# Optimization experiments

Hardware: AMD Instinct MI355X
Metric: run time of the kernel (lower is better)

## Reference

```python
import jax, jax.numpy as jnp
import numpy as np

N_NODES = 100000
N_EDGES = 3200000
STATE_DIM = 128
ACTION_DIM = 8


def _w(key, shape, scale=0.05):
    return (jax.random.normal(key, shape, dtype=jnp.float32) * scale)


def setup_inputs() -> dict:
    key = jax.random.key(0)
    ks = jax.random.split(key, 24)
    x = jax.random.normal(ks[0], (N_NODES, STATE_DIM), dtype=jnp.float32)
    edge_index = jax.random.randint(ks[1], (2, N_EDGES), 0, N_NODES, dtype=jnp.int64)
    inp = {
        "x": x,
        "edge_index": edge_index,
        # GCN layers (weights stored [in, out] so forward is x @ W + b)
        "W1": _w(ks[2], (STATE_DIM, 128)), "b1": jnp.zeros((128,), jnp.float32),
        "W2": _w(ks[3], (128, 128)),       "b2": jnp.zeros((128,), jnp.float32),
        "W3": _w(ks[4], (128, 64)),        "b3": jnp.zeros((64,), jnp.float32),
        # actor MLP 64->128->64->ACTION_DIM + softmax
        "Wa1": _w(ks[5], (64, 128)),  "ba1": jnp.zeros((128,), jnp.float32),
        "Wa2": _w(ks[6], (128, 64)),  "ba2": jnp.zeros((64,), jnp.float32),
        "Wa3": _w(ks[7], (64, ACTION_DIM)), "ba3": jnp.zeros((ACTION_DIM,), jnp.float32),
        # critic MLP 64->128->64->1
        "Wc1": _w(ks[8], (64, 128)),  "bc1": jnp.zeros((128,), jnp.float32),
        "Wc2": _w(ks[9], (128, 64)),  "bc2": jnp.zeros((64,), jnp.float32),
        "Wc3": _w(ks[10], (64, 1)),   "bc3": jnp.zeros((1,), jnp.float32),
    }
    return inp


def _gcn_conv(x, W, b, src, dst, norm):
    # GCNConv: D^{-1/2} (A + I) D^{-1/2} X W + b  (self loops already in src/dst)
    h = x @ W                                   # [N, out]
    msg = h[src] * norm[:, None]                # gather + per-edge scale
    agg = jax.ops.segment_sum(msg, dst, num_segments=N_NODES)
    return agg + b


def reference(x, edge_index,
              W1, b1, W2, b2, W3, b3,
              Wa1, ba1, Wa2, ba2, Wa3, ba3,
              Wc1, bc1, Wc2, bc2, Wc3, bc3):
    loop = jnp.arange(N_NODES, dtype=edge_index.dtype)
    src = jnp.concatenate([edge_index[0], loop])
    dst = jnp.concatenate([edge_index[1], loop])
    deg = jax.ops.segment_sum(jnp.ones_like(dst, dtype=x.dtype), dst,
                              num_segments=N_NODES)
    dinv = jax.lax.rsqrt(deg)                   # deg >= 1 via self loops
    norm = dinv[src] * dinv[dst]                # [E+N]

    # forward_gnn (dropout is identity in eval mode)
    h = jax.nn.relu(_gcn_conv(x, W1, b1, src, dst, norm))
    h = jax.nn.relu(_gcn_conv(h, W2, b2, src, dst, norm))
    h = _gcn_conv(h, W3, b3, src, dst, norm)    # [N, 64]

    a = jax.nn.relu(h @ Wa1 + ba1)
    a = jax.nn.relu(a @ Wa2 + ba2)
    probs = jax.nn.softmax(a @ Wa3 + ba3, axis=-1)   # [N, ACTION_DIM]

    c = jax.nn.relu(h @ Wc1 + bc1)
    c = jax.nn.relu(c @ Wc2 + bc2)
    values = c @ Wc3 + bc3                      # [N, 1]

    return jnp.concatenate([probs, values], axis=-1)  # [N, ACTION_DIM+1]
```

## Files before the change

kernel.cpp:

```cpp
#include <hip/hip_runtime.h>
#include <hip/hip_bf16.h>
#include <math.h>


#define WS_ALIGN(x) (((x) + 255) & ~(size_t)255)

constexpr int RNG    = 8;
constexpr int CHK    = 32;
constexpr int NRG_SZ = 12500;
constexpr int NB_A   = 256;

constexpr float S_FP8     = 64.0f;
constexpr float S_FP8_INV = 1.0f / 64.0f;

using bf16x8 = __attribute__((ext_vector_type(8))) short;
using f32x4  = __attribute__((ext_vector_type(4))) float;
using f32x2  = __attribute__((ext_vector_type(2))) float;

__device__ __forceinline__ float b2f(unsigned short u) {
    return __uint_as_float(((unsigned int)u) << 16);
}
__device__ __forceinline__ unsigned short f2b(float f) {
    __hip_bfloat16 hb = __float2bfloat16(f);
    return *(unsigned short*)&hb;
}
__device__ __forceinline__ unsigned char f2fp8(float f) {
    return (unsigned char)(__builtin_amdgcn_cvt_pk_fp8_f32(f, f, 0, false) & 0xff);
}
__device__ __forceinline__ int pad8(int v) { return (v + 7) & ~7; }


__global__ __launch_bounds__(256) void bucket_count_k(
    const int* __restrict__ dst, int* __restrict__ bcnt, int E) {
    __shared__ int c8[RNG];
    int b = blockIdx.x, t = threadIdx.x;
    if (t < RNG) c8[t] = 0;
    __syncthreads();
    int ec = (E + NB_A - 1) / NB_A;
    int e0 = b * ec, e1 = min(E, e0 + ec);
    for (int e = e0 + t; e < e1; e += 256) {
        int d = __builtin_nontemporal_load(dst + e);
        atomicAdd(&c8[d / NRG_SZ], 1);
    }
    __syncthreads();
    if (t < RNG) bcnt[t * NB_A + b] = c8[t];
}

__global__ void bucket_off_k(const int* __restrict__ bcnt, int* __restrict__ base,
                             int* __restrict__ bstart, int E) {
    __shared__ int s[RNG * NB_A];
    int t = threadIdx.x;
    s[t] = bcnt[t];
    s[t + 1024] = bcnt[t + 1024];
    __syncthreads();
    if (t == 0) {
        int run = 0;
        for (int i = 0; i < RNG * NB_A; i++) { int v = s[i]; s[i] = run; run += v; }
    }
    __syncthreads();
    base[t] = s[t];
    base[t + 1024] = s[t + 1024];
    if (t < RNG) bstart[t] = s[t * NB_A];
    if (t == 0) bstart[RNG] = E;
}

__global__ __launch_bounds__(256) void bucket_scatter_k(
    const int* __restrict__ src, const int* __restrict__ dst,
    const int* __restrict__ base, unsigned long long* __restrict__ bucket, int E) {
    __shared__ int cur[RNG];
    int b = blockIdx.x, t = threadIdx.x;
    if (t < RNG) cur[t] = base[t * NB_A + b];
    __syncthreads();
    int ec = (E + NB_A - 1) / NB_A;
    int e0 = b * ec, e1 = min(E, e0 + ec);
    for (int e = e0 + t; e < e1; e += 256) {
        int d = __builtin_nontemporal_load(dst + e);
        int sv = __builtin_nontemporal_load(src + e);
        int r = d / NRG_SZ;
        int pos = atomicAdd(&cur[r], 1);
        bucket[pos] = ((unsigned long long)(d - r * NRG_SZ) << 32) | (unsigned int)sv;
    }
}

__global__ __launch_bounds__(256) void hist_bucket_k(
    const unsigned long long* __restrict__ bucket, const int* __restrict__ bstart,
    int* __restrict__ hist) {
    __shared__ int h[NRG_SZ];
    int b = blockIdx.x, r = b & 7, c2 = b >> 3, t = threadIdx.x;
    for (int i = t; i < NRG_SZ; i += 256) h[i] = 0;
    int s0 = bstart[r], s1 = bstart[r + 1];
    int ec = (s1 - s0 + CHK - 1) / CHK;
    int e0 = s0 + c2 * ec, e1 = min(s1, e0 + ec);
    __syncthreads();
    for (int e = e0 + t; e < e1; e += 256) {
        unsigned long long v = __builtin_nontemporal_load(bucket + e);
        atomicAdd(&h[(int)(v >> 32)], 1);
    }
    __syncthreads();
    int* out = hist + ((size_t)r * CHK + c2) * NRG_SZ;
    for (int i = t; i < NRG_SZ; i += 256) out[i] = h[i];
}

__global__ void sum_hist_dinv_k(const int* __restrict__ hist, int* __restrict__ cnt,
                                float* __restrict__ dinv, int N) {
    int i = blockIdx.x * 256 + threadIdx.x;
    if (i >= N) return;
    int r = i / NRG_SZ, li = i - r * NRG_SZ;
    const int* hp = hist + ((size_t)r * CHK) * NRG_SZ + li;
    int s = 0;
#pragma unroll
    for (int c = 0; c < CHK; c++) s += hp[(size_t)c * NRG_SZ];
    cnt[i] = s;
    dinv[i] = rsqrtf((float)s + 1.0f);
}

__global__ void chunk_sum_k(const int* __restrict__ cnt, int* __restrict__ bsum, int n) {
    __shared__ int sd[256];
    int t = threadIdx.x;
    int i = blockIdx.x * 256 + t;
    sd[t] = (i < n) ? pad8(cnt[i]) : 0;
    __syncthreads();
    for (int d = 128; d > 0; d >>= 1) {
        if (t < d) sd[t] += sd[t + d];
        __syncthreads();
    }
    if (t == 0) bsum[blockIdx.x] = sd[0];
}

__global__ void scan_mid_k(const int* __restrict__ bsum, int* __restrict__ boff,
                           int nb, int* __restrict__ rowptr, int N) {
    __shared__ int s[512];
    int t = threadIdx.x;
    s[t] = (t < nb) ? bsum[t] : 0;
    __syncthreads();
    if (t == 0) {
        int run = 0;
        for (int i = 0; i < nb; i++) { int v = s[i]; s[i] = run; run += v; }
        rowptr[N] = run;
    }
    __syncthreads();
    if (t < nb) boff[t] = s[t];
}

__global__ void scan_final_k(const int* __restrict__ cnt, const int* __restrict__ boff,
                             int* __restrict__ rowptr, int n) {
    __shared__ int s[256];
    int t = threadIdx.x;
    int i = blockIdx.x * 256 + t;
    int v = (i < n) ? pad8(cnt[i]) : 0;
    s[t] = v;
    __syncthreads();
    for (int d = 1; d < 256; d <<= 1) {
        int x = (t >= d) ? s[t - d] : 0;
        __syncthreads();
        s[t] += x;
        __syncthreads();
    }
    if (i < n) rowptr[i] = s[t] - v + boff[blockIdx.x];
}

__global__ void offsets_k(int* __restrict__ hist, const int* __restrict__ rowptr, int N) {
    int i = blockIdx.x * 256 + threadIdx.x;
    if (i >= N) return;
    int r = i / NRG_SZ, li = i - r * NRG_SZ;
    int* hp = hist + ((size_t)r * CHK) * NRG_SZ + li;
    int run = rowptr[i];
#pragma unroll
    for (int c = 0; c < CHK; c++) {
        int v = hp[(size_t)c * NRG_SZ];
        hp[(size_t)c * NRG_SZ] = run;
        run += v;
    }
}

__global__ __launch_bounds__(256) void fill2_k(
    const unsigned long long* __restrict__ bucket, const int* __restrict__ bstart,
    const int* __restrict__ hist, int* __restrict__ col) {
    __shared__ int cur[NRG_SZ];
    int b = blockIdx.x, r = b & 7, c2 = b >> 3, t = threadIdx.x;
    const int* hp = hist + ((size_t)r * CHK + c2) * NRG_SZ;
    for (int i = t; i < NRG_SZ; i += 256) cur[i] = hp[i];
    int s0 = bstart[r], s1 = bstart[r + 1];
    int ec = (s1 - s0 + CHK - 1) / CHK;
    int e0 = s0 + c2 * ec, e1 = min(s1, e0 + ec);
    __syncthreads();
    for (int e = e0 + t; e < e1; e += 256) {
        unsigned long long v = __builtin_nontemporal_load(bucket + e);
        int slot = atomicAdd(&cur[(int)(v >> 32)], 1);
        col[slot] = (int)(unsigned int)(v & 0xffffffffULL);
    }
}

__global__ void pad_col_k(const int* __restrict__ cnt, const int* __restrict__ rowptr,
                          int* __restrict__ col, int N) {
    int i = blockIdx.x * 256 + threadIdx.x;
    if (i >= N) return;
    int e = rowptr[i] + cnt[i], end = rowptr[i + 1];
    for (; e < end; e++) col[e] = N;
}


__global__ __launch_bounds__(256) void prep_w_k(
    const float* __restrict__ W1, const float* __restrict__ W2,
    const float* __restrict__ W3, const float* __restrict__ Wa1,
    const float* __restrict__ Wa2, const float* __restrict__ Wc1,
    const float* __restrict__ Wc2, unsigned short* __restrict__ wt) {
    int i = blockIdx.x * 256 + threadIdx.x;
    const float* W; int off, K, OUT;
    if (i < 16384)      { W = W1;  off = 0;     K = 128; OUT = 128; }
    else if (i < 32768) { W = W2;  off = 16384; K = 128; OUT = 128; }
    else if (i < 40960) { W = W3;  off = 32768; K = 128; OUT = 64; }
    else if (i < 49152) { W = Wa1; off = 40960; K = 64;  OUT = 128; }
    else if (i < 57344) { W = Wa2; off = 49152; K = 128; OUT = 64; }
    else if (i < 65536) { W = Wc1; off = 57344; K = 64;  OUT = 128; }
    else                { W = Wc2; off = 65536; K = 128; OUT = 64; }
    int j = i - off, k = j / OUT, n = j - k * OUT;
    wt[off + n * K + k] = f2b(W[j]);
}


template <int K, int OUT, bool AF32, bool BIAS_RELU, bool OFP8>
__global__ __launch_bounds__(256) void gemm_mfma_k(
    const void* __restrict__ Xv, const unsigned short* __restrict__ Wt,
    const float* __restrict__ sb,
    void* __restrict__ Yv, int N) {
    constexpr int LDK = K + 8;
    __shared__ __align__(16) unsigned short As[64 * LDK];
    __shared__ __align__(16) unsigned short Bs[OUT * LDK];
    int t = threadIdx.x;
    int rowBase = blockIdx.x * 64;

    if constexpr (AF32) {
        const float* X = (const float*)Xv;
        for (int g = t; g < 64 * (K / 8); g += 256) {
            int r = g / (K / 8), q = g - r * (K / 8);
            int gr = rowBase + r;
            unsigned short us[8];
            if (gr < N) {
                float4 v0 = *(const float4*)(X + (size_t)gr * K + q * 8);
                float4 v1 = *(const float4*)(X + (size_t)gr * K + q * 8 + 4);
                us[0] = f2b(v0.x); us[1] = f2b(v0.y); us[2] = f2b(v0.z); us[3] = f2b(v0.w);
                us[4] = f2b(v1.x); us[5] = f2b(v1.y); us[6] = f2b(v1.z); us[7] = f2b(v1.w);
            } else {
#pragma unroll
                for (int j = 0; j < 8; j++) us[j] = 0;
            }
            *(uint4*)&As[r * LDK + q * 8] = *(uint4*)us;
        }
    } else {
        const unsigned short* X = (const unsigned short*)Xv;
        for (int g = t; g < 64 * (K / 8); g += 256) {
            int r = g / (K / 8), q = g - r * (K / 8);
            int gr = rowBase + r;
            uint4 v = make_uint4(0, 0, 0, 0);
            if (gr < N) v = *(const uint4*)(X + (size_t)gr * K + q * 8);
            *(uint4*)&As[r * LDK + q * 8] = v;
        }
    }
    for (int g = t; g < OUT * (K / 8); g += 256) {
        int r = g / (K / 8), q = g - r * (K / 8);
        *(uint4*)&Bs[r * LDK + q * 8] = *(const uint4*)(Wt + r * K + q * 8);
    }
    __syncthreads();

    int wv = t >> 6, lane = t & 63;
    int lm = lane & 15, lq = lane >> 4;
    constexpr int CT = OUT / 16;
    f32x4 acc[CT];
#pragma unroll
    for (int c = 0; c < CT; c++) acc[c] = (f32x4){0.f, 0.f, 0.f, 0.f};

    const unsigned short* arow = &As[(wv * 16 + lm) * LDK + lq * 8];
#pragma unroll
    for (int kt = 0; kt < K / 32; kt++) {
        bf16x8 a = *(const bf16x8*)(arow + kt * 32);
#pragma unroll
        for (int c = 0; c < CT; c++) {
            bf16x8 b = *(const bf16x8*)&Bs[(c * 16 + lm) * LDK + kt * 32 + lq * 8];
            acc[c] = __builtin_amdgcn_mfma_f32_16x16x32_bf16(a, b, acc[c], 0, 0, 0);
        }
    }

    int r0 = rowBase + wv * 16 + lq * 4;
#pragma unroll
    for (int r = 0; r < 4; r++) {
        int gr = r0 + r;
        if constexpr (OFP8) {
            float scale = (gr < N) ? sb[gr] * S_FP8 : 0.f;
#pragma unroll
            for (int c = 0; c < CT; c++) {
                int colg = c * 16 + lm;
                ((unsigned char*)Yv)[(size_t)gr * OUT + colg] = f2fp8(acc[c][r] * scale);
            }
        } else if (gr < N) {
#pragma unroll
            for (int c = 0; c < CT; c++) {
                int colg = c * 16 + lm;
                float v = acc[c][r];
                if constexpr (BIAS_RELU) v = fmaxf(v + sb[colg], 0.f);
                else v = v * sb[gr];
                ((unsigned short*)Yv)[(size_t)gr * OUT + colg] = f2b(v);
            }
        }
    }
}


template <bool RELU>
__global__ __launch_bounds__(256) void agg128_k(
    const unsigned char* __restrict__ H,
    const int* __restrict__ rowptr, const int* __restrict__ col,
    const float* __restrict__ dinv, const float* __restrict__ bias,
    unsigned short* __restrict__ Y, int N, int Ecap) {
    int tid = threadIdx.x;
    int node = blockIdx.x * 4 + (tid >> 6);
    if (node >= N) return;
    int lane = tid & 63;
    int half = lane >> 5;
    int li4 = (lane & 31) * 4;

    float acc0 = 0.f, acc1 = 0.f, acc2 = 0.f, acc3 = 0.f;
    if (half == 0) {
        unsigned u = *(const unsigned*)(H + (size_t)node * 128 + li4);
        f32x2 lo = __builtin_amdgcn_cvt_pk_f32_fp8((int)u, false);
        f32x2 hi = __builtin_amdgcn_cvt_pk_f32_fp8((int)u, true);
        acc0 = lo[0]; acc1 = lo[1]; acc2 = hi[0]; acc3 = hi[1];
    }

    int start = rowptr[node], end = rowptr[node + 1];
    for (int e0 = start; e0 < end; e0 += 64) {
        int cidx = e0 + lane;
        int cv = col[min(cidx, Ecap - 1)];
        int pairs = min(64, end - e0) >> 1;
        for (int p = 0; p < pairs; p += 4) {
            int s0 = __shfl(cv, 2 * p + half, 64);
            int s1 = __shfl(cv, 2 * p + 2 + half, 64);
            int s2 = __shfl(cv, 2 * p + 4 + half, 64);
            int s3 = __shfl(cv, 2 * p + 6 + half, 64);
            unsigned u0 = *(const unsigned*)(H + (size_t)s0 * 128 + li4);
            unsigned u1 = *(const unsigned*)(H + (size_t)s1 * 128 + li4);
            unsigned u2 = *(const unsigned*)(H + (size_t)s2 * 128 + li4);
            unsigned u3 = *(const unsigned*)(H + (size_t)s3 * 128 + li4);
            f32x2 a0 = __builtin_amdgcn_cvt_pk_f32_fp8((int)u0, false);
            f32x2 b0 = __builtin_amdgcn_cvt_pk_f32_fp8((int)u0, true);
            f32x2 a1 = __builtin_amdgcn_cvt_pk_f32_fp8((int)u1, false);
            f32x2 b1 = __builtin_amdgcn_cvt_pk_f32_fp8((int)u1, true);
            f32x2 a2 = __builtin_amdgcn_cvt_pk_f32_fp8((int)u2, false);
            f32x2 b2 = __builtin_amdgcn_cvt_pk_f32_fp8((int)u2, true);
            f32x2 a3 = __builtin_amdgcn_cvt_pk_f32_fp8((int)u3, false);
            f32x2 b3 = __builtin_amdgcn_cvt_pk_f32_fp8((int)u3, true);
            acc0 += (a0[0] + a1[0]) + (a2[0] + a3[0]);
            acc1 += (a0[1] + a1[1]) + (a2[1] + a3[1]);
            acc2 += (b0[0] + b1[0]) + (b2[0] + b3[0]);
            acc3 += (b0[1] + b1[1]) + (b2[1] + b3[1]);
        }
    }

    acc0 += __shfl_xor(acc0, 32, 64);
    acc1 += __shfl_xor(acc1, 32, 64);
    acc2 += __shfl_xor(acc2, 32, 64);
    acc3 += __shfl_xor(acc3, 32, 64);

    if (half == 0) {
        float dv = dinv[node] * S_FP8_INV;
        float4 bb = *(const float4*)(bias + li4);
        float o0 = acc0 * dv + bb.x, o1 = acc1 * dv + bb.y;
        float o2 = acc2 * dv + bb.z, o3 = acc3 * dv + bb.w;
        if (RELU) {
            o0 = fmaxf(o0, 0.f); o1 = fmaxf(o1, 0.f);
            o2 = fmaxf(o2, 0.f); o3 = fmaxf(o3, 0.f);
        }
        ushort4 st = make_ushort4(f2b(o0), f2b(o1), f2b(o2), f2b(o3));
        *(ushort4*)(Y + (size_t)node * 128 + li4) = st;
    }
}

__global__ __launch_bounds__(256) void agg64_k(
    const unsigned char* __restrict__ H,
    const int* __restrict__ rowptr, const int* __restrict__ col,
    const float* __restrict__ dinv, const float* __restrict__ bias,
    unsigned short* __restrict__ Y, int N, int Ecap) {
    int tid = threadIdx.x;
    int node = blockIdx.x * 4 + (tid >> 6);
    if (node >= N) return;
    int lane = tid & 63;
    int quarter = lane >> 4;
    int li4 = (lane & 15) * 4;

    float acc0 = 0.f, acc1 = 0.f, acc2 = 0.f, acc3 = 0.f;
    if (quarter == 0) {
        unsigned u = *(const unsigned*)(H + (size_t)node * 64 + li4);
        f32x2 lo = __builtin_amdgcn_cvt_pk_f32_fp8((int)u, false);
        f32x2 hi = __builtin_amdgcn_cvt_pk_f32_fp8((int)u, true);
        acc0 = lo[0]; acc1 = lo[1]; acc2 = hi[0]; acc3 = hi[1];
    }

    int start = rowptr[node], end = rowptr[node + 1];
    for (int e0 = start; e0 < end; e0 += 64) {
        int cidx = e0 + lane;
        int cv = col[min(cidx, Ecap - 1)];
        int quads = min(64, end - e0) >> 2;
        for (int q = 0; q < quads; q += 2) {
            int s0 = __shfl(cv, 4 * q + quarter, 64);
            int s1 = __shfl(cv, 4 * q + 4 + quarter, 64);
            unsigned u0 = *(const unsigned*)(H + (size_t)s0 * 64 + li4);
            unsigned u1 = *(const unsigned*)(H + (size_t)s1 * 64 + li4);
            f32x2 a0 = __builtin_amdgcn_cvt_pk_f32_fp8((int)u0, false);
            f32x2 b0 = __builtin_amdgcn_cvt_pk_f32_fp8((int)u0, true);
            f32x2 a1 = __builtin_amdgcn_cvt_pk_f32_fp8((int)u1, false);
            f32x2 b1 = __builtin_amdgcn_cvt_pk_f32_fp8((int)u1, true);
            acc0 += a0[0] + a1[0];
            acc1 += a0[1] + a1[1];
            acc2 += b0[0] + b1[0];
            acc3 += b0[1] + b1[1];
        }
    }

    acc0 += __shfl_xor(acc0, 16, 64); acc0 += __shfl_xor(acc0, 32, 64);
    acc1 += __shfl_xor(acc1, 16, 64); acc1 += __shfl_xor(acc1, 32, 64);
    acc2 += __shfl_xor(acc2, 16, 64); acc2 += __shfl_xor(acc2, 32, 64);
    acc3 += __shfl_xor(acc3, 16, 64); acc3 += __shfl_xor(acc3, 32, 64);

    if (quarter == 0 && (lane >> 5) == 0) {
        float dv = dinv[node] * S_FP8_INV;
        float4 bb = *(const float4*)(bias + li4);
        ushort4 st = make_ushort4(f2b(acc0 * dv + bb.x), f2b(acc1 * dv + bb.y),
                                  f2b(acc2 * dv + bb.z), f2b(acc3 * dv + bb.w));
        *(ushort4*)(Y + (size_t)node * 64 + li4) = st;
    }
}


__global__ __launch_bounds__(256) void logits_k(
    const unsigned short* __restrict__ A2,
    const unsigned short* __restrict__ C2,
    const float* __restrict__ Wa3, const float* __restrict__ ba3,
    const float* __restrict__ Wc3, const float* __restrict__ bc3,
    float* __restrict__ out, int N) {
    int t = threadIdx.x;
    int node = blockIdx.x * 32 + (t >> 3);
    int a = t & 7;
    if (node >= N) return;

    const unsigned short* ar = A2 + (size_t)node * 64;
    float s = ba3[a];
#pragma unroll
    for (int q = 0; q < 8; q++) {
        uint4 pv = *(const uint4*)(ar + q * 8);
        const unsigned short* pu = (const unsigned short*)&pv;
#pragma unroll
        for (int j = 0; j < 8; j++)
            s = fmaf(b2f(pu[j]), Wa3[(q * 8 + j) * 8 + a], s);
    }
    float m = s;
#pragma unroll
    for (int w = 1; w < 8; w <<= 1) m = fmaxf(m, __shfl_xor(m, w, 64));
    float e = expf(s - m);
    float sum = e;
#pragma unroll
    for (int w = 1; w < 8; w <<= 1) sum += __shfl_xor(sum, w, 64);
    out[(size_t)node * 9 + a] = e / sum;

    if (a == 0) {
        const unsigned short* cr = C2 + (size_t)node * 64;
        float v = bc3[0];
#pragma unroll
        for (int q = 0; q < 8; q++) {
            uint4 pv = *(const uint4*)(cr + q * 8);
            const unsigned short* pu = (const unsigned short*)&pv;
#pragma unroll
            for (int j = 0; j < 8; j++)
                v = fmaf(b2f(pu[j]), Wc3[q * 8 + j], v);
        }
        out[(size_t)node * 9 + 8] = v;
    }
}


extern "C" void kernel_launch(void* const* d_in, const int* in_sizes, int n_in,
                              void* d_out, int out_size, void* d_ws, size_t ws_size,
                              hipStream_t stream) {
    const float* x   = (const float*)d_in[0];
    const int*   ei  = (const int*)d_in[1];
    const float* W1  = (const float*)d_in[2];  const float* b1  = (const float*)d_in[3];
    const float* W2  = (const float*)d_in[4];  const float* b2  = (const float*)d_in[5];
    const float* W3  = (const float*)d_in[6];  const float* b3  = (const float*)d_in[7];
    const float* Wa1 = (const float*)d_in[8];  const float* ba1 = (const float*)d_in[9];
    const float* Wa2 = (const float*)d_in[10]; const float* ba2 = (const float*)d_in[11];
    const float* Wa3 = (const float*)d_in[12]; const float* ba3 = (const float*)d_in[13];
    const float* Wc1 = (const float*)d_in[14]; const float* bc1 = (const float*)d_in[15];
    const float* Wc2 = (const float*)d_in[16]; const float* bc2 = (const float*)d_in[17];
    const float* Wc3 = (const float*)d_in[18]; const float* bc3 = (const float*)d_in[19];
    float* out = (float*)d_out;

    const int N = in_sizes[0] / 128;
    const int E = in_sizes[1] / 2;
    const int* src = ei;
    const int* dst = ei + E;
    const int Ecap = E + 8 * N;
    const int Npad = ((N + 63) / 64) * 64;

    size_t off = 0;
    auto take = [&](size_t bytes) { size_t o = off; off = WS_ALIGN(off + bytes); return o; };
    char* ws = (char*)d_ws;
    unsigned short* h      = (unsigned short*)(ws + take((size_t)N * 128 * 2));
    unsigned char*  hpr8   = (unsigned char*) (ws + take((size_t)(Npad + 64) * 128));
    unsigned short* h3     = (unsigned short*)(ws + take((size_t)N * 64 * 2));
    int*            col    = (int*)(ws + take((size_t)Ecap * 4));
    unsigned short* A1C1   = (unsigned short*)(ws + take((size_t)N * 128 * 2));
    unsigned short* wt     = (unsigned short*)(ws + take(73728 * 2));
    float* dinv   = (float*)(ws + take((size_t)(N + 64) * 4));
    int*   cnt    = (int*)  (ws + take((size_t)N * 4));
    int*   rowptr = (int*)  (ws + take((size_t)(N + 1) * 4));
    int*   bcnt   = (int*)  (ws + take(RNG * NB_A * 4));
    int*   base   = (int*)  (ws + take(RNG * NB_A * 4));
    int*   bstart = (int*)  (ws + take((RNG + 1) * 4));
    int*   bsum   = (int*)  (ws + take(512 * 4));
    int*   boff   = (int*)  (ws + take(512 * 4));
    unsigned long long* bucket = (unsigned long long*)h;
    int* hist = (int*)A1C1;
    unsigned short* A2 = (unsigned short*)col;
    unsigned short* C2 = (unsigned short*)hpr8;
    (void)ws_size; (void)n_in; (void)out_size;

    const int nb  = (N + 255) / 256;
    const int gN  = (N + 255) / 256;
    const int gT  = (N + 63) / 64;

    prep_w_k<<<288, 256, 0, stream>>>(W1, W2, W3, Wa1, Wa2, Wc1, Wc2, wt);
    const unsigned short* W1t  = wt;
    const unsigned short* W2t  = wt + 16384;
    const unsigned short* W3t  = wt + 32768;
    const unsigned short* Wa1t = wt + 40960;
    const unsigned short* Wa2t = wt + 49152;
    const unsigned short* Wc1t = wt + 57344;
    const unsigned short* Wc2t = wt + 65536;

    bucket_count_k<<<NB_A, 256, 0, stream>>>(dst, bcnt, E);
    bucket_off_k<<<1, 1024, 0, stream>>>(bcnt, base, bstart, E);
    bucket_scatter_k<<<NB_A, 256, 0, stream>>>(src, dst, base, bucket, E);
    hist_bucket_k<<<RNG * CHK, 256, 0, stream>>>(bucket, bstart, hist);
    sum_hist_dinv_k<<<gN, 256, 0, stream>>>(hist, cnt, dinv, N);
    chunk_sum_k<<<nb, 256, 0, stream>>>(cnt, bsum, N);
    scan_mid_k<<<1, 512, 0, stream>>>(bsum, boff, nb, rowptr, N);
    scan_final_k<<<nb, 256, 0, stream>>>(cnt, boff, rowptr, N);
    offsets_k<<<gN, 256, 0, stream>>>(hist, rowptr, N);
    fill2_k<<<RNG * CHK, 256, 0, stream>>>(bucket, bstart, hist, col);
    pad_col_k<<<gN, 256, 0, stream>>>(cnt, rowptr, col, N);

    gemm_mfma_k<128, 128, true,  false, true><<<gT, 256, 0, stream>>>(x, W1t, dinv, hpr8, N);
    agg128_k<true><<<(N + 3) / 4, 256, 0, stream>>>(hpr8, rowptr, col, dinv, b1, h, N, Ecap);
    gemm_mfma_k<128, 128, false, false, true><<<gT, 256, 0, stream>>>(h, W2t, dinv, hpr8, N);
    agg128_k<true><<<(N + 3) / 4, 256, 0, stream>>>(hpr8, rowptr, col, dinv, b2, h, N, Ecap);
    gemm_mfma_k<128, 64,  false, false, true><<<gT, 256, 0, stream>>>(h, W3t, dinv, hpr8, N);
    agg64_k<<<(N + 3) / 4, 256, 0, stream>>>(hpr8, rowptr, col, dinv, b3, h3, N, Ecap);

    gemm_mfma_k<64,  128, false, true, false><<<gT, 256, 0, stream>>>(h3, Wa1t, ba1, A1C1, N);
    gemm_mfma_k<128, 64,  false, true, false><<<gT, 256, 0, stream>>>(A1C1, Wa2t, ba2, A2, N);
    gemm_mfma_k<64,  128, false, true, false><<<gT, 256, 0, stream>>>(h3, Wc1t, bc1, A1C1, N);
    gemm_mfma_k<128, 64,  false, true, false><<<gT, 256, 0, stream>>>(A1C1, Wc2t, bc2, C2, N);
    logits_k<<<(N + 31) / 32, 256, 0, stream>>>(A2, C2, Wa3, ba3, Wc3, bc3, out, N);
}
```

Baseline: 558.8 us.

## Use finer 64-range CSR bucketing with packed 32-bit keys and wider aggregation loads

```diff
diff --git a/kernel.cpp b/kernel.cpp
--- a/kernel.cpp
+++ b/kernel.cpp
@@ -5,10 +5,10 @@
 
 #define WS_ALIGN(x) (((x) + 255) & ~(size_t)255)
 
-constexpr int RNG    = 8;
-constexpr int CHK    = 32;
-constexpr int NRG_SZ = 12500;
-constexpr int NB_A   = 256;
+constexpr int RNG  = 64;
+constexpr int NRG  = 1563;
+constexpr int NB   = 1024;
+constexpr int CHK  = 16;
 
 constexpr float S_FP8     = 64.0f;
 constexpr float S_FP8_INV = 1.0f / 64.0f;
@@ -29,87 +29,109 @@
 }
 __device__ __forceinline__ int pad8(int v) { return (v + 7) & ~7; }
 
+__device__ __forceinline__ void acc8(uint2 u, f32x2& a01, f32x2& a23,
+                                     f32x2& a45, f32x2& a67) {
+    a01 += __builtin_amdgcn_cvt_pk_f32_fp8((int)u.x, false);
+    a23 += __builtin_amdgcn_cvt_pk_f32_fp8((int)u.x, true);
+    a45 += __builtin_amdgcn_cvt_pk_f32_fp8((int)u.y, false);
+    a67 += __builtin_amdgcn_cvt_pk_f32_fp8((int)u.y, true);
+}
+
 
 __global__ __launch_bounds__(256) void bucket_count_k(
     const int* __restrict__ dst, int* __restrict__ bcnt, int E) {
-    __shared__ int c8[RNG];
+    __shared__ int c64[RNG];
     int b = blockIdx.x, t = threadIdx.x;
-    if (t < RNG) c8[t] = 0;
-    __syncthreads();
-    int ec = (E + NB_A - 1) / NB_A;
+    if (t < RNG) c64[t] = 0;
+    __syncthreads();
+    int ec = (E + NB - 1) / NB;
     int e0 = b * ec, e1 = min(E, e0 + ec);
     for (int e = e0 + t; e < e1; e += 256) {
         int d = __builtin_nontemporal_load(dst + e);
-        atomicAdd(&c8[d / NRG_SZ], 1);
-    }
-    __syncthreads();
-    if (t < RNG) bcnt[t * NB_A + b] = c8[t];
-}
-
-__global__ void bucket_off_k(const int* __restrict__ bcnt, int* __restrict__ base,
-                             int* __restrict__ bstart, int E) {
-    __shared__ int s[RNG * NB_A];
-    int t = threadIdx.x;
-    s[t] = bcnt[t];
-    s[t + 1024] = bcnt[t + 1024];
-    __syncthreads();
-    if (t == 0) {
+        atomicAdd(&c64[d / NRG], 1);
+    }
+    __syncthreads();
+    if (t < RNG) bcnt[t * NB + b] = c64[t];
+}
+
+__global__ __launch_bounds__(256) void rsum_k(
+    const int* __restrict__ bcnt, int* __restrict__ base, int* __restrict__ rtot) {
+    __shared__ int s[256];
+    int r = blockIdx.x, t = threadIdx.x;
+    const int* row = bcnt + (size_t)r * NB;
+    int v[4], loc = 0;
+#pragma unroll
+    for (int j = 0; j < 4; j++) { v[j] = row[t * 4 + j]; loc += v[j]; }
+    s[t] = loc;
+    __syncthreads();
+    for (int d = 1; d < 256; d <<= 1) {
+        int x = (t >= d) ? s[t - d] : 0;
+        __syncthreads();
+        s[t] += x;
+        __syncthreads();
+    }
+    int run = s[t] - loc;
+    int* bp = base + (size_t)r * NB + t * 4;
+#pragma unroll
+    for (int j = 0; j < 4; j++) { bp[j] = run; run += v[j]; }
+    if (t == 255) rtot[r] = s[255];
+}
+
+__global__ void rstart_k(const int* __restrict__ rtot, int* __restrict__ bstart) {
+    if (threadIdx.x == 0) {
         int run = 0;
-        for (int i = 0; i < RNG * NB_A; i++) { int v = s[i]; s[i] = run; run += v; }
-    }
-    __syncthreads();
-    base[t] = s[t];
-    base[t + 1024] = s[t + 1024];
-    if (t < RNG) bstart[t] = s[t * NB_A];
-    if (t == 0) bstart[RNG] = E;
+        for (int r = 0; r < RNG; r++) { bstart[r] = run; run += rtot[r]; }
+        bstart[RNG] = run;
+    }
 }
 
 __global__ __launch_bounds__(256) void bucket_scatter_k(
     const int* __restrict__ src, const int* __restrict__ dst,
-    const int* __restrict__ base, unsigned long long* __restrict__ bucket, int E) {
+    const int* __restrict__ base, const int* __restrict__ bstart,
+    unsigned* __restrict__ bucket, int E) {
     __shared__ int cur[RNG];
     int b = blockIdx.x, t = threadIdx.x;
-    if (t < RNG) cur[t] = base[t * NB_A + b];
-    __syncthreads();
-    int ec = (E + NB_A - 1) / NB_A;
+    if (t < RNG) cur[t] = bstart[t] + base[(size_t)t * NB + b];
+    __syncthreads();
+    int ec = (E + NB - 1) / NB;
     int e0 = b * ec, e1 = min(E, e0 + ec);
     for (int e = e0 + t; e < e1; e += 256) {
         int d = __builtin_nontemporal_load(dst + e);
         int sv = __builtin_nontemporal_load(src + e);
-        int r = d / NRG_SZ;
+        int r = d / NRG;
         int pos = atomicAdd(&cur[r], 1);
-        bucket[pos] = ((unsigned long long)(d - r * NRG_SZ) << 32) | (unsigned int)sv;
+        bucket[pos] = ((unsigned)(d - r * NRG) << 17) | (unsigned)sv;
     }
 }
 
 __global__ __launch_bounds__(256) void hist_bucket_k(
-    const unsigned long long* __restrict__ bucket, const int* __restrict__ bstart,
+    const unsigned* __restrict__ bucket, const int* __restrict__ bstart,
     int* __restrict__ hist) {
-    __shared__ int h[NRG_SZ];
-    int b = blockIdx.x, r = b & 7, c2 = b >> 3, t = threadIdx.x;
-    for (int i = t; i < NRG_SZ; i += 256) h[i] = 0;
+    __shared__ int h[NRG];
+    int b = blockIdx.x, r = b & 63, c2 = b >> 6, t = threadIdx.x;
+    for (int i = t; i < NRG; i += 256) h[i] = 0;
     int s0 = bstart[r], s1 = bstart[r + 1];
     int ec = (s1 - s0 + CHK - 1) / CHK;
     int e0 = s0 + c2 * ec, e1 = min(s1, e0 + ec);
     __syncthreads();
     for (int e = e0 + t; e < e1; e += 256) {
-        unsigned long long v = __builtin_nontemporal_load(bucket + e);
-        atomicAdd(&h[(int)(v >> 32)], 1);
-    }
-    __syncthreads();
-    int* out = hist + ((size_t)r * CHK + c2) * NRG_SZ;
-    for (int i = t; i < NRG_SZ; i += 256) out[i] = h[i];
+        unsigned v = __builtin_nontemporal_load(bucket + e);
+        atomicAdd(&h[v >> 17], 1);
+    }
+    __syncthreads();
+    int* out = hist + ((size_t)r * CHK + c2) * NRG;
+    for (int i = t; i < NRG; i += 256) out[i] = h[i];
 }
 
 __global__ void sum_hist_dinv_k(const int* __restrict__ hist, int* __restrict__ cnt,
                                 float* __restrict__ dinv, int N) {
     int i = blockIdx.x * 256 + threadIdx.x;
     if (i >= N) return;
-    int r = i / NRG_SZ, li = i - r * NRG_SZ;
-    const int* hp = hist + ((size_t)r * CHK) * NRG_SZ + li;
+    int r = i / NRG, li = i - r * NRG;
+    const int* hp = hist + ((size_t)r * CHK) * NRG + li;
     int s = 0;
 #pragma unroll
-    for (int c = 0; c < CHK; c++) s += hp[(size_t)c * NRG_SZ];
+    for (int c = 0; c < CHK; c++) s += hp[(size_t)c * NRG];
     cnt[i] = s;
     dinv[i] = rsqrtf((float)s + 1.0f);
 }
@@ -162,32 +184,32 @@
 __global__ void offsets_k(int* __restrict__ hist, const int* __restrict__ rowptr, int N) {
     int i = blockIdx.x * 256 + threadIdx.x;
     if (i >= N) return;
-    int r = i / NRG_SZ, li = i - r * NRG_SZ;
-    int* hp = hist + ((size_t)r * CHK) * NRG_SZ + li;
+    int r = i / NRG, li = i - r * NRG;
+    int* hp = hist + ((size_t)r * CHK) * NRG + li;
     int run = rowptr[i];
 #pragma unroll
     for (int c = 0; c < CHK; c++) {
-        int v = hp[(size_t)c * NRG_SZ];
-        hp[(size_t)c * NRG_SZ] = run;
+        int v = hp[(size_t)c * NRG];
+        hp[(size_t)c * NRG] = run;
         run += v;
     }
 }
 
 __global__ __launch_bounds__(256) void fill2_k(
-    const unsigned long long* __restrict__ bucket, const int* __restrict__ bstart,
+    const unsigned* __restrict__ bucket, const int* __restrict__ bstart,
     const int* __restrict__ hist, int* __restrict__ col) {
-    __shared__ int cur[NRG_SZ];
-    int b = blockIdx.x, r = b & 7, c2 = b >> 3, t = threadIdx.x;
-    const int* hp = hist + ((size_t)r * CHK + c2) * NRG_SZ;
-    for (int i = t; i < NRG_SZ; i += 256) cur[i] = hp[i];
+    __shared__ int cur[NRG];
+    int b = blockIdx.x, r = b & 63, c2 = b >> 6, t = threadIdx.x;
+    const int* hp = hist + ((size_t)r * CHK + c2) * NRG;
+    for (int i = t; i < NRG; i += 256) cur[i] = hp[i];
     int s0 = bstart[r], s1 = bstart[r + 1];
     int ec = (s1 - s0 + CHK - 1) / CHK;
     int e0 = s0 + c2 * ec, e1 = min(s1, e0 + ec);
     __syncthreads();
     for (int e = e0 + t; e < e1; e += 256) {
-        unsigned long long v = __builtin_nontemporal_load(bucket + e);
-        int slot = atomicAdd(&cur[(int)(v >> 32)], 1);
-        col[slot] = (int)(unsigned int)(v & 0xffffffffULL);
+        unsigned v = __builtin_nontemporal_load(bucket + e);
+        int slot = atomicAdd(&cur[v >> 17], 1);
+        col[slot] = (int)(v & 0x1FFFFu);
     }
 }
 
@@ -316,62 +338,52 @@
     int node = blockIdx.x * 4 + (tid >> 6);
     if (node >= N) return;
     int lane = tid & 63;
-    int half = lane >> 5;
-    int li4 = (lane & 31) * 4;
-
-    float acc0 = 0.f, acc1 = 0.f, acc2 = 0.f, acc3 = 0.f;
-    if (half == 0) {
-        unsigned u = *(const unsigned*)(H + (size_t)node * 128 + li4);
-        f32x2 lo = __builtin_amdgcn_cvt_pk_f32_fp8((int)u, false);
-        f32x2 hi = __builtin_amdgcn_cvt_pk_f32_fp8((int)u, true);
-        acc0 = lo[0]; acc1 = lo[1]; acc2 = hi[0]; acc3 = hi[1];
+    int grp = lane >> 4;
+    int li8 = (lane & 15) * 8;
+
+    f32x2 a01 = {0.f, 0.f}, a23 = {0.f, 0.f}, a45 = {0.f, 0.f}, a67 = {0.f, 0.f};
+    if (grp == 0) {
+        uint2 u = *(const uint2*)(H + (size_t)node * 128 + li8);
+        acc8(u, a01, a23, a45, a67);
     }
 
     int start = rowptr[node], end = rowptr[node + 1];
     for (int e0 = start; e0 < end; e0 += 64) {
-        int cidx = e0 + lane;
-        int cv = col[min(cidx, Ecap - 1)];
-        int pairs = min(64, end - e0) >> 1;
-        for (int p = 0; p < pairs; p += 4) {
-            int s0 = __shfl(cv, 2 * p + half, 64);
-            int s1 = __shfl(cv, 2 * p + 2 + half, 64);
-            int s2 = __shfl(cv, 2 * p + 4 + half, 64);
-            int s3 = __shfl(cv, 2 * p + 6 + half, 64);
-            unsigned u0 = *(const unsigned*)(H + (size_t)s0 * 128 + li4);
-            unsigned u1 = *(const unsigned*)(H + (size_t)s1 * 128 + li4);
-            unsigned u2 = *(const unsigned*)(H + (size_t)s2 * 128 + li4);
-            unsigned u3 = *(const unsigned*)(H + (size_t)s3 * 128 + li4);
-            f32x2 a0 = __builtin_amdgcn_cvt_pk_f32_fp8((int)u0, false);
-            f32x2 b0 = __builtin_amdgcn_cvt_pk_f32_fp8((int)u0, true);
-            f32x2 a1 = __builtin_amdgcn_cvt_pk_f32_fp8((int)u1, false);
-            f32x2 b1 = __builtin_amdgcn_cvt_pk_f32_fp8((int)u1, true);
-            f32x2 a2 = __builtin_amdgcn_cvt_pk_f32_fp8((int)u2, false);
-            f32x2 b2 = __builtin_amdgcn_cvt_pk_f32_fp8((int)u2, true);
-            f32x2 a3 = __builtin_amdgcn_cvt_pk_f32_fp8((int)u3, false);
-            f32x2 b3 = __builtin_amdgcn_cvt_pk_f32_fp8((int)u3, true);
-            acc0 += (a0[0] + a1[0]) + (a2[0] + a3[0]);
-            acc1 += (a0[1] + a1[1]) + (a2[1] + a3[1]);
-            acc2 += (b0[0] + b1[0]) + (b2[0] + b3[0]);
-            acc3 += (b0[1] + b1[1]) + (b2[1] + b3[1]);
-        }
-    }
-
-    acc0 += __shfl_xor(acc0, 32, 64);
-    acc1 += __shfl_xor(acc1, 32, 64);
-    acc2 += __shfl_xor(acc2, 32, 64);
-    acc3 += __shfl_xor(acc3, 32, 64);
-
-    if (half == 0) {
+        int cv = col[min(e0 + lane, Ecap - 1)];
+        int quads = min(64, end - e0) >> 2;
+        for (int q = 0; q < quads; q += 2) {
+            int s0 = __shfl(cv, 4 * q + grp, 64);
+            int s1 = __shfl(cv, 4 * q + 4 + grp, 64);
+            uint2 u0 = *(const uint2*)(H + (size_t)s0 * 128 + li8);
+            uint2 u1 = *(const uint2*)(H + (size_t)s1 * 128 + li8);
+            acc8(u0, a01, a23, a45, a67);
+            acc8(u1, a01, a23, a45, a67);
+        }
+    }
+
+#pragma unroll
+    for (int w = 16; w < 64; w <<= 1) {
+        a01[0] += __shfl_xor(a01[0], w, 64); a01[1] += __shfl_xor(a01[1], w, 64);
+        a23[0] += __shfl_xor(a23[0], w, 64); a23[1] += __shfl_xor(a23[1], w, 64);
+        a45[0] += __shfl_xor(a45[0], w, 64); a45[1] += __shfl_xor(a45[1], w, 64);
+        a67[0] += __shfl_xor(a67[0], w, 64); a67[1] += __shfl_xor(a67[1], w, 64);
+    }
+
+    if (grp == 0) {
         float dv = dinv[node] * S_FP8_INV;
-        float4 bb = *(const float4*)(bias + li4);
-        float o0 = acc0 * dv + bb.x, o1 = acc1 * dv + bb.y;
-        float o2 = acc2 * dv + bb.z, o3 = acc3 * dv + bb.w;
+        float4 b0 = *(const float4*)(bias + li8);
+        float4 b1 = *(const float4*)(bias + li8 + 4);
+        float o0 = a01[0] * dv + b0.x, o1 = a01[1] * dv + b0.y;
+        float o2 = a23[0] * dv + b0.z, o3 = a23[1] * dv + b0.w;
+        float o4 = a45[0] * dv + b1.x, o5 = a45[1] * dv + b1.y;
+        float o6 = a67[0] * dv + b1.z, o7 = a67[1] * dv + b1.w;
         if (RELU) {
-            o0 = fmaxf(o0, 0.f); o1 = fmaxf(o1, 0.f);
-            o2 = fmaxf(o2, 0.f); o3 = fmaxf(o3, 0.f);
-        }
-        ushort4 st = make_ushort4(f2b(o0), f2b(o1), f2b(o2), f2b(o3));
-        *(ushort4*)(Y + (size_t)node * 128 + li4) = st;
+            o0 = fmaxf(o0, 0.f); o1 = fmaxf(o1, 0.f); o2 = fmaxf(o2, 0.f); o3 = fmaxf(o3, 0.f);
+            o4 = fmaxf(o4, 0.f); o5 = fmaxf(o5, 0.f); o6 = fmaxf(o6, 0.f); o7 = fmaxf(o7, 0.f);
+        }
+        unsigned short us[8] = {f2b(o0), f2b(o1), f2b(o2), f2b(o3),
+                                f2b(o4), f2b(o5), f2b(o6), f2b(o7)};
+        *(uint4*)(Y + (size_t)node * 128 + li8) = *(uint4*)us;
     }
 }
 
@@ -384,49 +396,53 @@
     int node = blockIdx.x * 4 + (tid >> 6);
     if (node >= N) return;
     int lane = tid & 63;
-    int quarter = lane >> 4;
-    int li4 = (lane & 15) * 4;
-
-    float acc0 = 0.f, acc1 = 0.f, acc2 = 0.f, acc3 = 0.f;
-    if (quarter == 0) {
-        unsigned u = *(const unsigned*)(H + (size_t)node * 64 + li4);
-        f32x2 lo = __builtin_amdgcn_cvt_pk_f32_fp8((int)u, false);
-        f32x2 hi = __builtin_amdgcn_cvt_pk_f32_fp8((int)u, true);
-        acc0 = lo[0]; acc1 = lo[1]; acc2 = hi[0]; acc3 = hi[1];
+    int grp = lane >> 3;
+    int li8 = (lane & 7) * 8;
+
+    f32x2 a01 = {0.f, 0.f}, a23 = {0.f, 0.f}, a45 = {0.f, 0.f}, a67 = {0.f, 0.f};
+    if (grp == 0) {
+        uint2 u = *(const uint2*)(H + (size_t)node * 64 + li8);
+        acc8(u, a01, a23, a45, a67);
     }
 
     int start = rowptr[node], end = rowptr[node + 1];
     for (int e0 = start; e0 < end; e0 += 64) {
-        int cidx = e0 + lane;
-        int cv = col[min(cidx, Ecap - 1)];
-        int quads = min(64, end - e0) >> 2;
-        for (int q = 0; q < quads; q += 2) {
-            int s0 = __shfl(cv, 4 * q + quarter, 64);
-            int s1 = __shfl(cv, 4 * q + 4 + quarter, 64);
-            unsigned u0 = *(const unsigned*)(H + (size_t)s0 * 64 + li4);
-            unsigned u1 = *(const unsigned*)(H + (size_t)s1 * 64 + li4);
-            f32x2 a0 = __builtin_amdgcn_cvt_pk_f32_fp8((int)u0, false);
-            f32x2 b0 = __builtin_amdgcn_cvt_pk_f32_fp8((int)u0, true);
-            f32x2 a1 = __builtin_amdgcn_cvt_pk_f32_fp8((int)u1, false);
-            f32x2 b1 = __builtin_amdgcn_cvt_pk_f32_fp8((int)u1, true);
-            acc0 += a0[0] + a1[0];
-            acc1 += a0[1] + a1[1];
-            acc2 += b0[0] + b1[0];
-            acc3 += b0[1] + b1[1];
-        }
-    }
-
-    acc0 += __shfl_xor(acc0, 16, 64); acc0 += __shfl_xor(acc0, 32, 64);
-    acc1 += __shfl_xor(acc1, 16, 64); acc1 += __shfl_xor(acc1, 32, 64);
-    acc2 += __shfl_xor(acc2, 16, 64); acc2 += __shfl_xor(acc2, 32, 64);
-    acc3 += __shfl_xor(acc3, 16, 64); acc3 += __shfl_xor(acc3, 32, 64);
-
-    if (quarter == 0 && (lane >> 5) == 0) {
+        int cv = col[min(e0 + lane, Ecap - 1)];
+        int octs = min(64, end - e0) >> 3;
+        int o = 0;
+        for (; o + 2 <= octs; o += 2) {
+            int s0 = __shfl(cv, 8 * o + grp, 64);
+            int s1 = __shfl(cv, 8 * o + 8 + grp, 64);
+            uint2 u0 = *(const uint2*)(H + (size_t)s0 * 64 + li8);
+            uint2 u1 = *(const uint2*)(H + (size_t)s1 * 64 + li8);
+            acc8(u0, a01, a23, a45, a67);
+            acc8(u1, a01, a23, a45, a67);
+        }
+        if (o < octs) {
+            int s0 = __shfl(cv, 8 * o + grp, 64);
+            uint2 u0 = *(const uint2*)(H + (size_t)s0 * 64 + li8);
+            acc8(u0, a01, a23, a45, a67);
+        }
+    }
+
+#pragma unroll
+    for (int w = 8; w < 64; w <<= 1) {
+        a01[0] += __shfl_xor(a01[0], w, 64); a01[1] += __shfl_xor(a01[1], w, 64);
+        a23[0] += __shfl_xor(a23[0], w, 64); a23[1] += __shfl_xor(a23[1], w, 64);
+        a45[0] += __shfl_xor(a45[0], w, 64); a45[1] += __shfl_xor(a45[1], w, 64);
+        a67[0] += __shfl_xor(a67[0], w, 64); a67[1] += __shfl_xor(a67[1], w, 64);
+    }
+
+    if (grp == 0) {
         float dv = dinv[node] * S_FP8_INV;
-        float4 bb = *(const float4*)(bias + li4);
-        ushort4 st = make_ushort4(f2b(acc0 * dv + bb.x), f2b(acc1 * dv + bb.y),
-                                  f2b(acc2 * dv + bb.z), f2b(acc3 * dv + bb.w));
-        *(ushort4*)(Y + (size_t)node * 64 + li4) = st;
+        float4 b0 = *(const float4*)(bias + li8);
+        float4 b1 = *(const float4*)(bias + li8 + 4);
+        unsigned short us[8] = {
+            f2b(a01[0] * dv + b0.x), f2b(a01[1] * dv + b0.y),
+            f2b(a23[0] * dv + b0.z), f2b(a23[1] * dv + b0.w),
+            f2b(a45[0] * dv + b1.x), f2b(a45[1] * dv + b1.y),
+            f2b(a67[0] * dv + b1.z), f2b(a67[1] * dv + b1.w)};
+        *(uint4*)(Y + (size_t)node * 64 + li8) = *(uint4*)us;
     }
 }
 
@@ -512,12 +528,13 @@
     float* dinv   = (float*)(ws + take((size_t)(N + 64) * 4));
     int*   cnt    = (int*)  (ws + take((size_t)N * 4));
     int*   rowptr = (int*)  (ws + take((size_t)(N + 1) * 4));
-    int*   bcnt   = (int*)  (ws + take(RNG * NB_A * 4));
-    int*   base   = (int*)  (ws + take(RNG * NB_A * 4));
+    int*   bcnt   = (int*)  (ws + take((size_t)RNG * NB * 4));
+    int*   base   = (int*)  (ws + take((size_t)RNG * NB * 4));
+    int*   rtot   = (int*)  (ws + take(RNG * 4));
     int*   bstart = (int*)  (ws + take((RNG + 1) * 4));
     int*   bsum   = (int*)  (ws + take(512 * 4));
     int*   boff   = (int*)  (ws + take(512 * 4));
-    unsigned long long* bucket = (unsigned long long*)h;
+    unsigned* bucket = (unsigned*)h;
     int* hist = (int*)A1C1;
     unsigned short* A2 = (unsigned short*)col;
     unsigned short* C2 = (unsigned short*)hpr8;
@@ -536,9 +553,10 @@
     const unsigned short* Wc1t = wt + 57344;
     const unsigned short* Wc2t = wt + 65536;
 
-    bucket_count_k<<<NB_A, 256, 0, stream>>>(dst, bcnt, E);
-    bucket_off_k<<<1, 1024, 0, stream>>>(bcnt, base, bstart, E);
-    bucket_scatter_k<<<NB_A, 256, 0, stream>>>(src, dst, base, bucket, E);
+    bucket_count_k<<<NB, 256, 0, stream>>>(dst, bcnt, E);
+    rsum_k<<<RNG, 256, 0, stream>>>(bcnt, base, rtot);
+    rstart_k<<<1, 64, 0, stream>>>(rtot, bstart);
+    bucket_scatter_k<<<NB, 256, 0, stream>>>(src, dst, base, bstart, bucket, E);
     hist_bucket_k<<<RNG * CHK, 256, 0, stream>>>(bucket, bstart, hist);
     sum_hist_dinv_k<<<gN, 256, 0, stream>>>(hist, cnt, dinv, N);
     chunk_sum_k<<<nb, 256, 0, stream>>>(cnt, bsum, N);
```

Measured after the change: 507.0 us. -9.3%, faster.
